# Optimization experiments

Hardware: AMD Instinct MI355X
Metric: run time of the kernel (lower is better)

Reference implementation:

```python
import jax, jax.numpy as jnp
import numpy as np

N = 100000
E = 640000
D_IN = 128
D_OUT = 128


def setup_inputs() -> dict:
    key = jax.random.key(0)
    k1, k2, k3, k4, k5 = jax.random.split(key, 5)
    x = jax.random.normal(k1, (N, D_IN), dtype=jnp.float32)
    edge_index = jax.random.randint(k2, (2, E), 0, N, dtype=jnp.int64)
    edge_weight = jax.random.uniform(k3, (E,), dtype=jnp.float32)
    W_rel = jax.random.normal(k4, (D_OUT, D_IN), dtype=jnp.float32) / np.sqrt(D_IN)
    W_root = jax.random.normal(k5, (D_OUT, D_IN), dtype=jnp.float32) / np.sqrt(D_IN)
    b = jnp.zeros((D_OUT,), dtype=jnp.float32)
    return {"x": x, "edge_index": edge_index, "edge_weight": edge_weight,
            "W_rel": W_rel, "W_root": W_root, "b": b}


def reference(x, edge_index, edge_weight, W_rel, W_root, b):
    # PyG GraphConv: out_i = W_rel @ (sum_{j -> i} w_ij * x_j) + W_root @ x_i + b
    src = edge_index[0]  # message source (x_j)
    dst = edge_index[1]  # aggregation target
    msg = x[src] * edge_weight[:, None]          # [E, D_IN] gather + scale
    agg = jax.ops.segment_sum(msg, dst, num_segments=x.shape[0])  # [N, D_IN]
    out = agg @ W_rel.T + x @ W_root.T + b       # [N, D_OUT]
    return out
```

## Files before the change

### kernel.cpp

```cpp
#include <hip/hip_runtime.h>
#include <hip/hip_fp16.h>

#define NN 100000
#define EE 640000
#define D 128
#define NBINS NN
#define SCAN_NBLK 98

#define CSTRIDE 100352
#define OSTRIDE 100032

#define WS_CNT8     0
#define WS_OFFSX    802816
#define WS_BSUM     1603072
#define WS_ESLOT    1603200
#define WS_SW       2243200
#define WS_WF       3523200
#define WS_XH       3539584
#define WS_INTS_TOP 9939584

#define WS_CNT      0
#define WS_OFFS     100000
#define WS_BSUMM    200000
#define WS_SWM      200192
#define WS_WCONV    1480192
#define WS_INTS_MID 1512960

#define PREP_XB 3125
#define PREP_WB 128
#define PREP_HB 2500

typedef __attribute__((ext_vector_type(8))) short    short8v;
typedef __attribute__((ext_vector_type(8))) _Float16 half8v;
typedef __attribute__((ext_vector_type(4))) float    floatx4;
struct __align__(8) half4t { __half2 a, b; };

__device__ inline void split_bf16(float f, short& h, short& l) {
    unsigned u  = __float_as_uint(f);
    unsigned hb = u & 0xFFFF0000u;
    h = (short)(u >> 16);
    float fl = f - __uint_as_float(hb);
    l = (short)(__float_as_uint(fl) >> 16);
}

__global__ __launch_bounds__(256) void scatter_kernel(
    const float* __restrict__ x, const int* __restrict__ ei,
    const float* __restrict__ ew, float* agg)
{
    int gid = blockIdx.x * 256 + threadIdx.x;
    int e = gid >> 7, f = gid & 127;
    if (e >= EE) return;
    float v = x[ei[e] * D + f] * ew[e];
    unsafeAtomicAdd(&agg[ei[EE + e] * D + f], v);
}

__global__ __launch_bounds__(256) void zero8_kernel(int* __restrict__ cnt8)
{
    int i = blockIdx.x * 256 + threadIdx.x;
    if (i < 8 * CSTRIDE) cnt8[i] = 0;
}

__global__ __launch_bounds__(256) void zero_cnt_kernel(int* __restrict__ cnt)
{
    int i = blockIdx.x * 256 + threadIdx.x;
    if (i < NBINS) cnt[i] = 0;
}

__global__ __launch_bounds__(256) void prep_kernel(
    const float* __restrict__ x, const float* __restrict__ Wrel,
    const float* __restrict__ Wroot, const int* __restrict__ ei,
    short* __restrict__ xh, short* __restrict__ Wf,
    int* __restrict__ cnt8, int* __restrict__ eslot)
{
    const int b = blockIdx.x;
    if (b < PREP_XB) {
        const int base = b * 4096 + threadIdx.x * 4;
        float4 v[4];
        #pragma unroll
        for (int u = 0; u < 4; u++)
            v[u] = *(const float4*)&x[base + u * 1024];
        #pragma unroll
        for (int u = 0; u < 4; u++) {
            short4 h;
            h.x = (short)__half_as_ushort(__float2half(v[u].x));
            h.y = (short)__half_as_ushort(__float2half(v[u].y));
            h.z = (short)__half_as_ushort(__float2half(v[u].z));
            h.w = (short)__half_as_ushort(__float2half(v[u].w));
            *(short4*)&xh[base + u * 1024] = h;
        }
    } else if (b < PREP_XB + PREP_WB) {
        int i = (b - PREP_XB) * 256 + threadIdx.x;
        int c = i >> 8, k = i & 255;
        float f = (k < 128) ? Wrel[c * 128 + k] : Wroot[c * 128 + (k - 128)];
        Wf[i] = (short)__half_as_ushort(__float2half(f));
    } else {
        int e = (b - PREP_XB - PREP_WB) * 256 + threadIdx.x;
        if (e < EE) {
            int dst  = ei[EE + e];
            int cp   = b & 7;
            int slot = atomicAdd(&cnt8[cp * CSTRIDE + dst], 1);
            eslot[e] = (slot << 3) | cp;
        }
    }
}

__global__ __launch_bounds__(256) void scanA8_kernel(
    const int* __restrict__ cnt8, int* __restrict__ offsx, int* __restrict__ bsum)
{
    __shared__ int tsum[256];
    const int tid = threadIdx.x;
    const int base = blockIdx.x * 1024 + tid * 4;
    int v[4], pc[8][4];
    int s = 0;
    #pragma unroll
    for (int i = 0; i < 4; i++) {
        int bin = base + i;
        int run = 0;
        #pragma unroll
        for (int cp = 0; cp < 8; cp++) {
            int cv = (bin < NBINS) ? cnt8[cp * CSTRIDE + bin] : 0;
            pc[cp][i] = run;
            run += cv;
        }
        v[i] = run;
        s += run;
    }
    tsum[tid] = s;
    __syncthreads();
    for (int off = 1; off < 256; off <<= 1) {
        int t = (tid >= off) ? tsum[tid - off] : 0;
        __syncthreads();
        tsum[tid] += t;
        __syncthreads();
    }
    int run = tsum[tid] - s;
    #pragma unroll
    for (int i = 0; i < 4; i++) {
        int bin = base + i;
        if (bin < NBINS) {
            #pragma unroll
            for (int cp = 0; cp < 8; cp++)
                offsx[cp * OSTRIDE + bin] = run + pc[cp][i];
        }
        run += v[i];
    }
    if (tid == 255) bsum[blockIdx.x] = tsum[255];
}

__global__ __launch_bounds__(256) void scanC8_kernel(
    int* __restrict__ offsx, const int* __restrict__ bsum)
{
    __shared__ int s[128];
    const int tid = threadIdx.x;
    if (tid < 128) s[tid] = (tid < SCAN_NBLK) ? bsum[tid] : 0;
    __syncthreads();
    for (int off = 1; off < 128; off <<= 1) {
        int t = 0;
        if (tid < 128 && tid >= off) t = s[tid - off];
        __syncthreads();
        if (tid < 128) s[tid] += t;
        __syncthreads();
    }
    const int add = (blockIdx.x == 0) ? 0 : s[blockIdx.x - 1];
    const int base = blockIdx.x * 1024 + tid * 4;
    #pragma unroll
    for (int i = 0; i < 4; i++) {
        int bin = base + i;
        if (bin < NBINS) {
            #pragma unroll
            for (int cp = 0; cp < 8; cp++)
                offsx[cp * OSTRIDE + bin] += add;
        }
    }
    if (blockIdx.x == 0 && tid == 0) offsx[NN] = EE;
}

__global__ __launch_bounds__(256) void build_kernel(
    const int* __restrict__ ei, const float* __restrict__ ew,
    const int* __restrict__ offsx, const int* __restrict__ eslot,
    int2* __restrict__ sw)
{
    int e = blockIdx.x * 256 + threadIdx.x;
    if (e >= EE) return;
    int dst = ei[EE + e];
    int es  = eslot[e];
    int p   = offsx[(es & 7) * OSTRIDE + dst] + (es >> 3);
    sw[p] = make_int2(ei[e], __float_as_int(ew[e]));
}

__global__ __launch_bounds__(256) void aggregate_h_kernel(
    const short* __restrict__ xh, const int* __restrict__ offsx,
    const int2* __restrict__ sw, float* __restrict__ out)
{
    const int node = blockIdx.x * 8 + (threadIdx.x >> 5);
    const int fl   = threadIdx.x & 31;
    if (node >= NN) return;
    const int beg = offsx[node];
    const int end = offsx[node + 1];
    const half4t* xp = (const half4t*)xh;

    float4 a0 = make_float4(0.f, 0.f, 0.f, 0.f);
    float4 a1 = make_float4(0.f, 0.f, 0.f, 0.f);
    int j = beg;
    for (; j + 3 < end; j += 4) {
        int2 s0 = sw[j], s1 = sw[j + 1], s2 = sw[j + 2], s3 = sw[j + 3];
        half4t v0 = xp[(size_t)s0.x * 32 + fl];
        half4t v1 = xp[(size_t)s1.x * 32 + fl];
        half4t v2 = xp[(size_t)s2.x * 32 + fl];
        half4t v3 = xp[(size_t)s3.x * 32 + fl];
        float w0 = __int_as_float(s0.y), w1 = __int_as_float(s1.y);
        float w2 = __int_as_float(s2.y), w3 = __int_as_float(s3.y);
        float2 l0 = __half22float2(v0.a), h0 = __half22float2(v0.b);
        float2 l1 = __half22float2(v1.a), h1 = __half22float2(v1.b);
        float2 l2 = __half22float2(v2.a), h2 = __half22float2(v2.b);
        float2 l3 = __half22float2(v3.a), h3 = __half22float2(v3.b);
        a0.x += w0 * l0.x; a0.y += w0 * l0.y; a0.z += w0 * h0.x; a0.w += w0 * h0.y;
        a1.x += w1 * l1.x; a1.y += w1 * l1.y; a1.z += w1 * h1.x; a1.w += w1 * h1.y;
        a0.x += w2 * l2.x; a0.y += w2 * l2.y; a0.z += w2 * h2.x; a0.w += w2 * h2.y;
        a1.x += w3 * l3.x; a1.y += w3 * l3.y; a1.z += w3 * h3.x; a1.w += w3 * h3.y;
    }
    for (; j + 1 < end; j += 2) {
        int2 s0 = sw[j], s1 = sw[j + 1];
        half4t v0 = xp[(size_t)s0.x * 32 + fl];
        half4t v1 = xp[(size_t)s1.x * 32 + fl];
        float w0 = __int_as_float(s0.y), w1 = __int_as_float(s1.y);
        float2 l0 = __half22float2(v0.a), h0 = __half22float2(v0.b);
        float2 l1 = __half22float2(v1.a), h1 = __half22float2(v1.b);
        a0.x += w0 * l0.x; a0.y += w0 * l0.y; a0.z += w0 * h0.x; a0.w += w0 * h0.y;
        a1.x += w1 * l1.x; a1.y += w1 * l1.y; a1.z += w1 * h1.x; a1.w += w1 * h1.y;
    }
    if (j < end) {
        int2 s0 = sw[j];
        half4t v0 = xp[(size_t)s0.x * 32 + fl];
        float w0 = __int_as_float(s0.y);
        float2 l0 = __half22float2(v0.a), h0 = __half22float2(v0.b);
        a0.x += w0 * l0.x; a0.y += w0 * l0.y; a0.z += w0 * h0.x; a0.w += w0 * h0.y;
    }
    float4 r = make_float4(a0.x + a1.x, a0.y + a1.y, a0.z + a1.z, a0.w + a1.w);
    half4t o;
    o.a = __floats2half2_rn(r.x, r.y);
    o.b = __floats2half2_rn(r.z, r.w);
    half4t* op = (half4t*)((char*)out + (size_t)node * 512 + 256);
    op[fl] = o;
}

__global__ __launch_bounds__(256) void mfma_f16_kernel(
    const short* __restrict__ xh, const short* __restrict__ Wf,
    const float* __restrict__ bias, float* __restrict__ out)
{
    __shared__ short lds[2 * 128 * 64];
    short* At = lds;
    short* Wt = lds + 8192;

    const int tid  = threadIdx.x;
    const int lane = tid & 63;
    const int wave = tid >> 6;
    const int row0 = blockIdx.x * 128;
    const int frow = lane & 15;

    floatx4 acc[2][8];
    #pragma unroll
    for (int nf = 0; nf < 8; nf++) {
        float b = bias[nf * 16 + frow];
        #pragma unroll
        for (int mf = 0; mf < 2; mf++) acc[mf][nf] = (floatx4){b, b, b, b};
    }

    const short* aggh = (const short*)out;

    for (int kc = 0; kc < 4; kc++) {
        __syncthreads();
        #pragma unroll
        for (int i = 0; i < 4; i++) {
            int e = (i * 256 + tid) * 8;
            int r = e >> 6, k = e & 63;
            int rg = row0 + r;
            short8v v = (short8v)0;
            if (rg < NN) {
                if (kc < 2) v = *(const short8v*)&aggh[(size_t)rg * 256 + 128 + kc * 64 + k];
                else        v = *(const short8v*)&xh[(size_t)rg * 128 + (kc - 2) * 64 + k];
            }
            int sidx = r * 64 + (((k >> 3) ^ (r & 7)) << 3);
            *(short8v*)&At[sidx] = v;
        }
        #pragma unroll
        for (int i = 0; i < 4; i++) {
            int e = (i * 256 + tid) * 8;
            int c = e >> 6, k = e & 63;
            int sidx = c * 64 + (((k >> 3) ^ (c & 7)) << 3);
            *(short8v*)&Wt[sidx] = *(const short8v*)&Wf[c * 256 + kc * 64 + k];
        }
        __syncthreads();

        const int arow = wave * 32;
        #pragma unroll
        for (int kf = 0; kf < 2; kf++) {
            const int kblk = kf * 4 + (lane >> 4);
            half8v a[2];
            #pragma unroll
            for (int mf = 0; mf < 2; mf++) {
                int r = arow + mf * 16 + frow;
                int idx = r * 64 + ((kblk ^ (r & 7)) << 3);
                a[mf] = *(const half8v*)&At[idx];
            }
            #pragma unroll
            for (int nf = 0; nf < 8; nf++) {
                int cc = nf * 16 + frow;
                int idx = cc * 64 + ((kblk ^ (cc & 7)) << 3);
                half8v b = *(const half8v*)&Wt[idx];
                #pragma unroll
                for (int mf = 0; mf < 2; mf++)
                    acc[mf][nf] = __builtin_amdgcn_mfma_f32_16x16x32_f16(a[mf], b, acc[mf][nf], 0, 0, 0);
            }
        }
    }

    const int orow = row0 + wave * 32;
    #pragma unroll
    for (int mf = 0; mf < 2; mf++) {
        #pragma unroll
        for (int j = 0; j < 4; j++) {
            int r = orow + mf * 16 + (lane >> 4) * 4 + j;
            if (r < NN) {
                #pragma unroll
                for (int nf = 0; nf < 8; nf++)
                    out[(size_t)r * D + nf * 16 + (lane & 15)] = acc[mf][nf][j];
            }
        }
    }
}

__global__ __launch_bounds__(256) void hist_kernel(
    const int* __restrict__ ei, int* __restrict__ cnt)
{
    int e = blockIdx.x * 256 + threadIdx.x;
    if (e < EE) atomicAdd(&cnt[ei[EE + e]], 1);
}

__global__ __launch_bounds__(256) void wconv_kernel(
    const float* __restrict__ Wrel, const float* __restrict__ Wroot,
    short* __restrict__ Wb)
{
    int i = blockIdx.x * 256 + threadIdx.x;
    int c = i >> 8, k = i & 255;
    float f = (k < 128) ? Wrel[c * 128 + k] : Wroot[c * 128 + (k - 128)];
    short h, l;
    split_bf16(f, h, l);
    Wb[i] = h;
    Wb[32768 + i] = l;
}

__global__ __launch_bounds__(256) void scanA_kernel(
    const int* __restrict__ cnt, int* __restrict__ offs, int* __restrict__ bsum)
{
    __shared__ int tsum[256];
    const int tid = threadIdx.x;
    const int base = blockIdx.x * 1024 + tid * 4;
    int v[4], s = 0;
    #pragma unroll
    for (int i = 0; i < 4; i++) {
        int idx = base + i;
        v[i] = (idx < NBINS) ? cnt[idx] : 0;
        s += v[i];
    }
    tsum[tid] = s;
    __syncthreads();
    for (int off = 1; off < 256; off <<= 1) {
        int t = (tid >= off) ? tsum[tid - off] : 0;
        __syncthreads();
        tsum[tid] += t;
        __syncthreads();
    }
    int run = tsum[tid] - s;
    #pragma unroll
    for (int i = 0; i < 4; i++) {
        int idx = base + i;
        if (idx < NBINS) offs[idx] = run;
        run += v[i];
    }
    if (tid == 255) bsum[blockIdx.x] = tsum[255];
}

__global__ __launch_bounds__(256) void scanC_kernel(
    int* __restrict__ offs, const int* __restrict__ bsum)
{
    __shared__ int s[128];
    const int tid = threadIdx.x;
    if (tid < 128) s[tid] = (tid < SCAN_NBLK) ? bsum[tid] : 0;
    __syncthreads();
    for (int off = 1; off < 128; off <<= 1) {
        int t = 0;
        if (tid < 128 && tid >= off) t = s[tid - off];
        __syncthreads();
        if (tid < 128) s[tid] += t;
        __syncthreads();
    }
    const int add = (blockIdx.x == 0) ? 0 : s[blockIdx.x - 1];
    const int base = blockIdx.x * 1024 + tid * 4;
    #pragma unroll
    for (int i = 0; i < 4; i++) {
        int idx = base + i;
        if (idx < NBINS) offs[idx] += add;
    }
}

__global__ __launch_bounds__(256) void buildM_kernel(
    const int* __restrict__ ei, const float* __restrict__ ew,
    int* __restrict__ offs, int2* __restrict__ sw)
{
    int e = blockIdx.x * 256 + threadIdx.x;
    if (e >= EE) return;
    int dst = ei[EE + e];
    int p = atomicAdd(&offs[dst], 1);
    sw[p] = make_int2(ei[e], __float_as_int(ew[e]));
}

__global__ __launch_bounds__(256) void aggregate_kernel(
    const float* __restrict__ x, const int* __restrict__ offs,
    const int2* __restrict__ sw, float* __restrict__ out)
{
    const int node = blockIdx.x * 8 + (threadIdx.x >> 5);
    const int fl   = threadIdx.x & 31;
    if (node >= NN) return;
    const int beg = (node == 0) ? 0 : offs[node - 1];
    const int end = offs[node];
    const float4* x4 = (const float4*)x;

    float4 a0 = make_float4(0.f, 0.f, 0.f, 0.f);
    float4 a1 = make_float4(0.f, 0.f, 0.f, 0.f);
    int j = beg;
    for (; j + 1 < end; j += 2) {
        int2 s0 = sw[j];
        int2 s1 = sw[j + 1];
        float4 v0 = x4[(size_t)s0.x * 32 + fl];
        float4 v1 = x4[(size_t)s1.x * 32 + fl];
        float w0 = __int_as_float(s0.y), w1 = __int_as_float(s1.y);
        a0.x += w0 * v0.x; a0.y += w0 * v0.y; a0.z += w0 * v0.z; a0.w += w0 * v0.w;
        a1.x += w1 * v1.x; a1.y += w1 * v1.y; a1.z += w1 * v1.z; a1.w += w1 * v1.w;
    }
    if (j < end) {
        int2 s0 = sw[j];
        float4 v0 = x4[(size_t)s0.x * 32 + fl];
        float w0 = __int_as_float(s0.y);
        a0.x += w0 * v0.x; a0.y += w0 * v0.y; a0.z += w0 * v0.z; a0.w += w0 * v0.w;
    }
    float4 r = make_float4(a0.x + a1.x, a0.y + a1.y, a0.z + a1.z, a0.w + a1.w);
    ((float4*)out)[(size_t)node * 32 + fl] = r;
}

__global__ __launch_bounds__(256) void mfma_gemm_kernel(
    const float* __restrict__ x, const short* __restrict__ Wb,
    const float* __restrict__ bias, float* __restrict__ out)
{
    __shared__ short lds[4 * 128 * 64];
    short* Ah = lds;
    short* Al = lds + 8192;
    short* Wh = lds + 16384;
    short* Wl = lds + 24576;

    const int tid  = threadIdx.x;
    const int lane = tid & 63;
    const int wave = tid >> 6;
    const int row0 = blockIdx.x * 128;
    const int frow = lane & 15;
    const int fk   = (lane >> 4) * 8;

    floatx4 acc[2][8];
    #pragma unroll
    for (int nf = 0; nf < 8; nf++) {
        float b = bias[nf * 16 + frow];
        #pragma unroll
        for (int mf = 0; mf < 2; mf++) acc[mf][nf] = (floatx4){b, b, b, b};
    }

    for (int kc = 0; kc < 4; kc++) {
        const float* A = (kc < 2) ? out : x;
        const int kcol = (kc & 1) * 64;
        __syncthreads();
        #pragma unroll
        for (int i = 0; i < 8; i++) {
            int e = (i * 256 + tid) * 4;
            int r = e >> 6, k = e & 63;
            int rg = row0 + r;
            float4 v = (rg < NN) ? *(const float4*)&A[(size_t)rg * D + kcol + k]
                                 : make_float4(0.f, 0.f, 0.f, 0.f);
            short4 h, l;
            split_bf16(v.x, h.x, l.x);
            split_bf16(v.y, h.y, l.y);
            split_bf16(v.z, h.z, l.z);
            split_bf16(v.w, h.w, l.w);
            int sidx = r * 64 + (((k >> 3) ^ (r & 7)) << 3) + (k & 7);
            *(short4*)&Ah[sidx] = h;
            *(short4*)&Al[sidx] = l;
        }
        #pragma unroll
        for (int i = 0; i < 4; i++) {
            int e = (i * 256 + tid) * 8;
            int c = e >> 6, k = e & 63;
            int sidx = c * 64 + (((k >> 3) ^ (c & 7)) << 3);
            int g = c * 256 + kc * 64 + k;
            *(short8v*)&Wh[sidx] = *(const short8v*)&Wb[g];
            *(short8v*)&Wl[sidx] = *(const short8v*)&Wb[32768 + g];
        }
        __syncthreads();

        const int arow = wave * 32;
        #pragma unroll
        for (int kf = 0; kf < 2; kf++) {
            const int kblk = (kf * 32 + fk) >> 3;
            short8v ah[2], al[2];
            #pragma unroll
            for (int mf = 0; mf < 2; mf++) {
                int r = arow + mf * 16 + frow;
                int idx = r * 64 + ((kblk ^ (r & 7)) << 3);
                ah[mf] = *(const short8v*)&Ah[idx];
                al[mf] = *(const short8v*)&Al[idx];
            }
            #pragma unroll
            for (int nf = 0; nf < 8; nf++) {
                int cc = nf * 16 + frow;
                int idx = cc * 64 + ((kblk ^ (cc & 7)) << 3);
                short8v bh = *(const short8v*)&Wh[idx];
                short8v bl = *(const short8v*)&Wl[idx];
                #pragma unroll
                for (int mf = 0; mf < 2; mf++) {
                    acc[mf][nf] = __builtin_amdgcn_mfma_f32_16x16x32_bf16(ah[mf], bh, acc[mf][nf], 0, 0, 0);
                    acc[mf][nf] = __builtin_amdgcn_mfma_f32_16x16x32_bf16(al[mf], bh, acc[mf][nf], 0, 0, 0);
                    acc[mf][nf] = __builtin_amdgcn_mfma_f32_16x16x32_bf16(ah[mf], bl, acc[mf][nf], 0, 0, 0);
                }
            }
        }
    }

    const int orow = row0 + wave * 32;
    #pragma unroll
    for (int mf = 0; mf < 2; mf++) {
        #pragma unroll
        for (int j = 0; j < 4; j++) {
            int r = orow + mf * 16 + (lane >> 4) * 4 + j;
            if (r < NN) {
                #pragma unroll
                for (int nf = 0; nf < 8; nf++)
                    out[(size_t)r * D + nf * 16 + (lane & 15)] = acc[mf][nf][j];
            }
        }
    }
}

__global__ __launch_bounds__(512) void gemm_kernel(
    const float* __restrict__ x, const float* __restrict__ Wrel,
    const float* __restrict__ Wroot, const float* __restrict__ bias,
    float* out)
{
    __shared__ float AtT[128][65];
    const int tid  = threadIdx.x;
    const int lane = tid & 63;
    const int wid  = __builtin_amdgcn_readfirstlane(tid >> 6);
    const int row0 = blockIdx.x * 64;
    float acc[16];
    {
        const float* bb = bias + wid * 16;
        #pragma unroll
        for (int c = 0; c < 16; c++) acc[c] = bb[c];
    }
    for (int phase = 0; phase < 2; phase++) {
        const float* A = phase ? x : out;
        const float* W = (phase ? Wroot : Wrel) + wid * 16 * D;
        __syncthreads();
        #pragma unroll
        for (int i = 0; i < 16; i++) {
            int e = i * 512 + tid;
            int r = e >> 7, k = e & 127;
            int rg = row0 + r;
            AtT[k][r] = (rg < NN) ? A[rg * D + k] : 0.0f;
        }
        __syncthreads();
        for (int k4 = 0; k4 < 32; k4++) {
            float a0 = AtT[k4 * 4 + 0][lane];
            float a1 = AtT[k4 * 4 + 1][lane];
            float a2 = AtT[k4 * 4 + 2][lane];
            float a3 = AtT[k4 * 4 + 3][lane];
            #pragma unroll
            for (int c = 0; c < 16; c++) {
                const float* wp = W + c * D + k4 * 4;
                acc[c] += a0 * wp[0] + a1 * wp[1] + a2 * wp[2] + a3 * wp[3];
            }
        }
    }
    __syncthreads();
    #pragma unroll
    for (int c = 0; c < 16; c++)
        AtT[wid * 16 + c][lane] = acc[c];
    __syncthreads();
    #pragma unroll
    for (int i = 0; i < 16; i++) {
        int e = i * 512 + tid;
        int r = e >> 7, col = e & 127;
        int rg = row0 + r;
        if (rg < NN) out[rg * D + col] = AtT[col][r];
    }
}

extern "C" void kernel_launch(void* const* d_in, const int* in_sizes, int n_in,
                              void* d_out, int out_size, void* d_ws, size_t ws_size,
                              hipStream_t stream) {
    const float* x     = (const float*)d_in[0];
    const int*   ei    = (const int*)  d_in[1];
    const float* ew    = (const float*)d_in[2];
    const float* Wrel  = (const float*)d_in[3];
    const float* Wroot = (const float*)d_in[4];
    const float* bias  = (const float*)d_in[5];
    float*       out   = (float*)d_out;

    const int eb = (EE + 255) / 256;

    if (ws_size >= (size_t)WS_INTS_TOP * sizeof(int)) {
        int* w = (int*)d_ws;
        int*   cnt8  = w + WS_CNT8;
        int*   offsx = w + WS_OFFSX;
        int*   bsum  = w + WS_BSUM;
        int*   eslot = w + WS_ESLOT;
        int2*  sw    = (int2*)(w + WS_SW);
        short* Wf    = (short*)(w + WS_WF);
        short* xh    = (short*)(w + WS_XH);

        zero8_kernel<<<(8 * CSTRIDE) / 256, 256, 0, stream>>>(cnt8);
        prep_kernel<<<PREP_XB + PREP_WB + PREP_HB, 256, 0, stream>>>(
            x, Wrel, Wroot, ei, xh, Wf, cnt8, eslot);
        scanA8_kernel<<<SCAN_NBLK, 256, 0, stream>>>(cnt8, offsx, bsum);
        scanC8_kernel<<<SCAN_NBLK, 256, 0, stream>>>(offsx, bsum);
        build_kernel<<<eb, 256, 0, stream>>>(ei, ew, offsx, eslot, sw);
        aggregate_h_kernel<<<NN / 8, 256, 0, stream>>>(xh, offsx, sw, out);
        mfma_f16_kernel<<<(NN + 127) / 128, 256, 0, stream>>>(xh, Wf, bias, out);
    } else if (ws_size >= (size_t)WS_INTS_MID * sizeof(int)) {
        int* w = (int*)d_ws;
        int*   cnt  = w + WS_CNT;
        int*   offs = w + WS_OFFS;
        int*   bsum = w + WS_BSUMM;
        int2*  sw   = (int2*)(w + WS_SWM);
        short* Wb   = (short*)(w + WS_WCONV);

        zero_cnt_kernel<<<(NBINS + 255) / 256, 256, 0, stream>>>(cnt);
        wconv_kernel<<<128, 256, 0, stream>>>(Wrel, Wroot, Wb);
        hist_kernel <<<eb, 256, 0, stream>>>(ei, cnt);
        scanA_kernel<<<SCAN_NBLK, 256, 0, stream>>>(cnt, offs, bsum);
        scanC_kernel<<<SCAN_NBLK, 256, 0, stream>>>(offs, bsum);
        buildM_kernel<<<eb, 256, 0, stream>>>(ei, ew, offs, sw);
        aggregate_kernel<<<NN / 8, 256, 0, stream>>>(x, offs, sw, out);
        mfma_gemm_kernel<<<(NN + 127) / 128, 256, 0, stream>>>(x, Wb, bias, out);
    } else {
        hipMemsetAsync(out, 0, (size_t)NN * D * sizeof(float), stream);
        scatter_kernel<<<(EE * 128) / 256, 256, 0, stream>>>(x, ei, ew, out);
        gemm_kernel<<<(NN + 63) / 64, 512, 0, stream>>>(x, Wrel, Wroot, bias, out);
    }
}
```

Measured before the change: 130.4 us.

## Replace stored edge slots with atomic cursor fill and split prep kernel

Stops the histogram pass from recording each edge's slot. The build pass now claims positions with atomicAdd on the partitioned offset array, and the scan writes a separate plain offset array for the aggregation. The fused prep kernel is split into separate x-conversion, weight-conversion and histogram kernels, and x conversion uses wider per-thread vector stores. This drops the eslot write and read traffic at the cost of a second round of atomics in the build pass, two extra launches, and a nondeterministic edge order within each node.

```diff
diff --git a/kernel.cpp b/kernel.cpp
--- a/kernel.cpp
+++ b/kernel.cpp
@@ -12,23 +12,19 @@
 
 #define WS_CNT8     0
 #define WS_OFFSX    802816
-#define WS_BSUM     1603072
-#define WS_ESLOT    1603200
-#define WS_SW       2243200
-#define WS_WF       3523200
-#define WS_XH       3539584
-#define WS_INTS_TOP 9939584
-
-#define WS_CNT      0
-#define WS_OFFS     100000
+#define WS_OFFS     1603072
+#define WS_BSUM     1703104
+#define WS_SW       1703232
+#define WS_WF       2983232
+#define WS_XH       2999616
+#define WS_INTS_TOP 9399616
+
+#define WS_CNTM     0
+#define WS_OFFSM    100000
 #define WS_BSUMM    200000
 #define WS_SWM      200192
 #define WS_WCONV    1480192
 #define WS_INTS_MID 1512960
-
-#define PREP_XB 3125
-#define PREP_WB 128
-#define PREP_HB 2500
 
 typedef __attribute__((ext_vector_type(8))) short    short8v;
 typedef __attribute__((ext_vector_type(8))) _Float16 half8v;
@@ -66,46 +62,58 @@
     if (i < NBINS) cnt[i] = 0;
 }
 
-__global__ __launch_bounds__(256) void prep_kernel(
-    const float* __restrict__ x, const float* __restrict__ Wrel,
-    const float* __restrict__ Wroot, const int* __restrict__ ei,
-    short* __restrict__ xh, short* __restrict__ Wf,
-    int* __restrict__ cnt8, int* __restrict__ eslot)
-{
-    const int b = blockIdx.x;
-    if (b < PREP_XB) {
-        const int base = b * 4096 + threadIdx.x * 4;
-        float4 v[4];
-        #pragma unroll
-        for (int u = 0; u < 4; u++)
-            v[u] = *(const float4*)&x[base + u * 1024];
-        #pragma unroll
-        for (int u = 0; u < 4; u++) {
-            short4 h;
-            h.x = (short)__half_as_ushort(__float2half(v[u].x));
-            h.y = (short)__half_as_ushort(__float2half(v[u].y));
-            h.z = (short)__half_as_ushort(__float2half(v[u].z));
-            h.w = (short)__half_as_ushort(__float2half(v[u].w));
-            *(short4*)&xh[base + u * 1024] = h;
-        }
-    } else if (b < PREP_XB + PREP_WB) {
-        int i = (b - PREP_XB) * 256 + threadIdx.x;
-        int c = i >> 8, k = i & 255;
-        float f = (k < 128) ? Wrel[c * 128 + k] : Wroot[c * 128 + (k - 128)];
-        Wf[i] = (short)__half_as_ushort(__float2half(f));
-    } else {
-        int e = (b - PREP_XB - PREP_WB) * 256 + threadIdx.x;
-        if (e < EE) {
-            int dst  = ei[EE + e];
-            int cp   = b & 7;
-            int slot = atomicAdd(&cnt8[cp * CSTRIDE + dst], 1);
-            eslot[e] = (slot << 3) | cp;
-        }
+__global__ __launch_bounds__(256) void xconv_kernel(
+    const float* __restrict__ x, short* __restrict__ xh)
+{
+    const int base = (blockIdx.x * 256 + threadIdx.x) * 16;
+    float4 v[4];
+    #pragma unroll
+    for (int u = 0; u < 4; u++)
+        v[u] = *(const float4*)&x[base + u * 4];
+    short8v h0, h1;
+    h0[0] = (short)__half_as_ushort(__float2half(v[0].x));
+    h0[1] = (short)__half_as_ushort(__float2half(v[0].y));
+    h0[2] = (short)__half_as_ushort(__float2half(v[0].z));
+    h0[3] = (short)__half_as_ushort(__float2half(v[0].w));
+    h0[4] = (short)__half_as_ushort(__float2half(v[1].x));
+    h0[5] = (short)__half_as_ushort(__float2half(v[1].y));
+    h0[6] = (short)__half_as_ushort(__float2half(v[1].z));
+    h0[7] = (short)__half_as_ushort(__float2half(v[1].w));
+    h1[0] = (short)__half_as_ushort(__float2half(v[2].x));
+    h1[1] = (short)__half_as_ushort(__float2half(v[2].y));
+    h1[2] = (short)__half_as_ushort(__float2half(v[2].z));
+    h1[3] = (short)__half_as_ushort(__float2half(v[2].w));
+    h1[4] = (short)__half_as_ushort(__float2half(v[3].x));
+    h1[5] = (short)__half_as_ushort(__float2half(v[3].y));
+    h1[6] = (short)__half_as_ushort(__float2half(v[3].z));
+    h1[7] = (short)__half_as_ushort(__float2half(v[3].w));
+    *(short8v*)&xh[base]     = h0;
+    *(short8v*)&xh[base + 8] = h1;
+}
+
+__global__ __launch_bounds__(256) void wf_kernel(
+    const float* __restrict__ Wrel, const float* __restrict__ Wroot,
+    short* __restrict__ Wf)
+{
+    int i = blockIdx.x * 256 + threadIdx.x;
+    int c = i >> 8, k = i & 255;
+    float f = (k < 128) ? Wrel[c * 128 + k] : Wroot[c * 128 + (k - 128)];
+    Wf[i] = (short)__half_as_ushort(__float2half(f));
+}
+
+__global__ __launch_bounds__(256) void histx_kernel(
+    const int* __restrict__ ei, int* __restrict__ cnt8)
+{
+    int e = blockIdx.x * 256 + threadIdx.x;
+    if (e < EE) {
+        int dst = ei[EE + e];
+        atomicAdd(&cnt8[(blockIdx.x & 7) * CSTRIDE + dst], 1);
     }
 }
 
 __global__ __launch_bounds__(256) void scanA8_kernel(
-    const int* __restrict__ cnt8, int* __restrict__ offsx, int* __restrict__ bsum)
+    const int* __restrict__ cnt8, int* __restrict__ offsx,
+    int* __restrict__ offs, int* __restrict__ bsum)
 {
     __shared__ int tsum[256];
     const int tid = threadIdx.x;
@@ -138,6 +146,7 @@
     for (int i = 0; i < 4; i++) {
         int bin = base + i;
         if (bin < NBINS) {
+            offs[bin] = run;
             #pragma unroll
             for (int cp = 0; cp < 8; cp++)
                 offsx[cp * OSTRIDE + bin] = run + pc[cp][i];
@@ -148,7 +157,7 @@
 }
 
 __global__ __launch_bounds__(256) void scanC8_kernel(
-    int* __restrict__ offsx, const int* __restrict__ bsum)
+    int* __restrict__ offsx, int* __restrict__ offs, const int* __restrict__ bsum)
 {
     __shared__ int s[128];
     const int tid = threadIdx.x;
@@ -167,36 +176,35 @@
     for (int i = 0; i < 4; i++) {
         int bin = base + i;
         if (bin < NBINS) {
+            offs[bin] += add;
             #pragma unroll
             for (int cp = 0; cp < 8; cp++)
                 offsx[cp * OSTRIDE + bin] += add;
         }
     }
-    if (blockIdx.x == 0 && tid == 0) offsx[NN] = EE;
-}
-
-__global__ __launch_bounds__(256) void build_kernel(
+    if (blockIdx.x == 0 && tid == 0) offs[NN] = EE;
+}
+
+__global__ __launch_bounds__(256) void buildx_kernel(
     const int* __restrict__ ei, const float* __restrict__ ew,
-    const int* __restrict__ offsx, const int* __restrict__ eslot,
-    int2* __restrict__ sw)
+    int* __restrict__ offsx, int2* __restrict__ sw)
 {
     int e = blockIdx.x * 256 + threadIdx.x;
     if (e >= EE) return;
     int dst = ei[EE + e];
-    int es  = eslot[e];
-    int p   = offsx[(es & 7) * OSTRIDE + dst] + (es >> 3);
+    int p = atomicAdd(&offsx[(blockIdx.x & 7) * OSTRIDE + dst], 1);
     sw[p] = make_int2(ei[e], __float_as_int(ew[e]));
 }
 
 __global__ __launch_bounds__(256) void aggregate_h_kernel(
-    const short* __restrict__ xh, const int* __restrict__ offsx,
+    const short* __restrict__ xh, const int* __restrict__ offs,
     const int2* __restrict__ sw, float* __restrict__ out)
 {
     const int node = blockIdx.x * 8 + (threadIdx.x >> 5);
     const int fl   = threadIdx.x & 31;
     if (node >= NN) return;
-    const int beg = offsx[node];
-    const int end = offsx[node + 1];
+    const int beg = offs[node];
+    const int end = offs[node + 1];
     const half4t* xp = (const half4t*)xh;
 
     float4 a0 = make_float4(0.f, 0.f, 0.f, 0.f);
@@ -618,24 +626,25 @@
         int* w = (int*)d_ws;
         int*   cnt8  = w + WS_CNT8;
         int*   offsx = w + WS_OFFSX;
+        int*   offs  = w + WS_OFFS;
         int*   bsum  = w + WS_BSUM;
-        int*   eslot = w + WS_ESLOT;
         int2*  sw    = (int2*)(w + WS_SW);
         short* Wf    = (short*)(w + WS_WF);
         short* xh    = (short*)(w + WS_XH);
 
         zero8_kernel<<<(8 * CSTRIDE) / 256, 256, 0, stream>>>(cnt8);
-        prep_kernel<<<PREP_XB + PREP_WB + PREP_HB, 256, 0, stream>>>(
-            x, Wrel, Wroot, ei, xh, Wf, cnt8, eslot);
-        scanA8_kernel<<<SCAN_NBLK, 256, 0, stream>>>(cnt8, offsx, bsum);
-        scanC8_kernel<<<SCAN_NBLK, 256, 0, stream>>>(offsx, bsum);
-        build_kernel<<<eb, 256, 0, stream>>>(ei, ew, offsx, eslot, sw);
-        aggregate_h_kernel<<<NN / 8, 256, 0, stream>>>(xh, offsx, sw, out);
+        xconv_kernel<<<(NN * D) / (256 * 16), 256, 0, stream>>>(x, xh);
+        wf_kernel<<<128, 256, 0, stream>>>(Wrel, Wroot, Wf);
+        histx_kernel<<<eb, 256, 0, stream>>>(ei, cnt8);
+        scanA8_kernel<<<SCAN_NBLK, 256, 0, stream>>>(cnt8, offsx, offs, bsum);
+        scanC8_kernel<<<SCAN_NBLK, 256, 0, stream>>>(offsx, offs, bsum);
+        buildx_kernel<<<eb, 256, 0, stream>>>(ei, ew, offsx, sw);
+        aggregate_h_kernel<<<NN / 8, 256, 0, stream>>>(xh, offs, sw, out);
         mfma_f16_kernel<<<(NN + 127) / 128, 256, 0, stream>>>(xh, Wf, bias, out);
     } else if (ws_size >= (size_t)WS_INTS_MID * sizeof(int)) {
         int* w = (int*)d_ws;
-        int*   cnt  = w + WS_CNT;
-        int*   offs = w + WS_OFFS;
+        int*   cnt  = w + WS_CNTM;
+        int*   offs = w + WS_OFFSM;
         int*   bsum = w + WS_BSUMM;
         int2*  sw   = (int2*)(w + WS_SWM);
         short* Wb   = (short*)(w + WS_WCONV);
```

After: 152.2 us. 1.17x slower.
